# Kernel tuning notes

Hardware: AMD Instinct MI355X
Metric: run time of the kernel (lower is better)

## Reference

```python
import jax, jax.numpy as jnp
import numpy as np
import math

B, TQ, TK = 64, 1024, 512
CONV_CH, EMBED_DIM, ATT_HID = 512, 512, 512
KEY_POS_RATE = 1.385
QUERY_POS_RATE = 1.0
POSITION_WEIGHT = 1.0


def sin_pos_enc(positions, w, d):
    # positions: [B, T] int, padding_idx=0 maps to zero vector.
    # pe[..., 2i]   = sin(w*pos / 10000^(2i/d))
    # pe[..., 2i+1] = cos(w*pos / 10000^(2i/d))
    i = jnp.arange(d)
    inv_freq = jnp.power(jnp.float32(10000.0), -(2.0 * (i // 2).astype(jnp.float32)) / d)  # [d]
    ang = (positions.astype(jnp.float32) * w)[..., None] * inv_freq  # [B, T, d]
    pe = jnp.where(i % 2 == 0, jnp.sin(ang), jnp.cos(ang))
    return jnp.where((positions == 0)[..., None], jnp.float32(0.0), pe)


def setup_inputs() -> dict:
    key = jax.random.key(0)
    ks = jax.random.split(key, 12)
    s = 0.02
    inp = {
        "query": jax.random.normal(ks[0], (B, TQ, CONV_CH), jnp.float32),
        "keys": jax.random.normal(ks[1], (B, TK, EMBED_DIM), jnp.float32),
        "values": jax.random.normal(ks[2], (B, TK, EMBED_DIM), jnp.float32),
        # 1-based positions (0 is the padding index of SinusoidalEncoding)
        "text_positions": jnp.broadcast_to(jnp.arange(1, TK + 1, dtype=jnp.int64), (B, TK)),
        "frame_positions": jnp.broadcast_to(jnp.arange(1, TQ + 1, dtype=jnp.int64), (B, TQ)),
        # pad mask over keys: last 64 text positions are padding
        "mask": jnp.broadcast_to(jnp.arange(TK) >= (TK - 64), (B, TK)),
        "Wq": jax.random.normal(ks[3], (CONV_CH, ATT_HID), jnp.float32) * s,
        "bq": jnp.zeros((ATT_HID,), jnp.float32),
        "Wk": jax.random.normal(ks[4], (EMBED_DIM, ATT_HID), jnp.float32) * s,
        "bk": jnp.zeros((ATT_HID,), jnp.float32),
        "Wv": jax.random.normal(ks[5], (EMBED_DIM, ATT_HID), jnp.float32) * s,
        "bv": jnp.zeros((ATT_HID,), jnp.float32),
        "Wo": jax.random.normal(ks[6], (ATT_HID, CONV_CH), jnp.float32) * s,
        "bo": jnp.zeros((CONV_CH,), jnp.float32),
    }
    return inp


def reference(query, keys, values, text_positions, frame_positions, mask,
              Wq, bq, Wk, bk, Wv, bv, Wo, bo):
    # positional-bias injection (position_weight = 1.0)
    keys = keys + POSITION_WEIGHT * sin_pos_enc(text_positions, KEY_POS_RATE, EMBED_DIM)[:, :keys.shape[1], :]
    query = query + POSITION_WEIGHT * sin_pos_enc(frame_positions, QUERY_POS_RATE, CONV_CH)[:, :frame_positions.shape[-1], :]

    v = values @ Wv + bv            # [B, TK, H]
    k = keys @ Wk + bk              # [B, TK, H]
    q = query @ Wq + bq             # [B, TQ, H]

    scores = jnp.einsum('bqh,bkh->bqk', q, k)               # [B, TQ, TK]
    scores = jnp.where(mask[:, None, :], -jnp.inf, scores)
    attn = jax.nn.softmax(scores, axis=2)
    # dropout is a no-op in eval mode
    x = jnp.einsum('bqk,bkh->bqh', attn, v)
    x = x * jnp.float32(math.sqrt(1.0 / v.shape[1]))
    out = x @ Wo + bo               # [B, TQ, conv_channels]
    return out, attn
```

## Files before the change

kernel.cpp:

```cpp
#include <hip/hip_runtime.h>
#include <stdint.h>

#define DEVI __device__ __forceinline__

typedef __attribute__((ext_vector_type(4))) float     f4v;
typedef __attribute__((ext_vector_type(8))) _Float16  h8;
typedef __attribute__((ext_vector_type(4))) _Float16  h4;
typedef unsigned int  u32;

static constexpr int   TQ = 1024, TKN = 512;
static constexpr float KEY_RATE = 1.385f;
static constexpr float QRY_RATE = 1.0f;
static constexpr float SCALE    = 0.04419417382415922f;
static constexpr float INVC     = 0.05190512648261504f;

static constexpr size_t OFF_MM   = 0;
static constexpr size_t OFF_NT   = OFF_MM  + (size_t)512*512*2;
static constexpr size_t OFF_WOT  = OFF_NT  + (size_t)512*512*2;
static constexpr size_t OFF_PEQ  = OFF_WOT + (size_t)512*512*4;
static constexpr size_t OFF_W    = OFF_PEQ + (size_t)1024*512*4;
static constexpr size_t OFF_C    = OFF_W   + 2048;
static constexpr size_t OFF_BQBK = OFF_C   + 2048;
static constexpr size_t OFF_T    = OFF_BQBK + 256;
static constexpr size_t OFF_KP   = OFF_T   + (size_t)64*512*4;
static constexpr size_t OFF_MKT  = OFF_KP  + (size_t)64*512*512*2;
static constexpr size_t OFF_PT   = OFF_MKT + (size_t)64*512*512*2;
static constexpr size_t WS_NEED  = OFF_PT  + (size_t)64*512*512*2;
static constexpr size_t OFF_A16  = WS_NEED;
static constexpr size_t WS_BIG   = OFF_A16 + (size_t)64*1024*512*2;

#define WAITV(N) asm volatile("s_waitcnt vmcnt(" #N ")" ::: "memory")
#define WAITL()  asm volatile("s_waitcnt lgkmcnt(0)" ::: "memory")
#define SCHEDB() __builtin_amdgcn_sched_barrier(0)
#define BARRAW() __builtin_amdgcn_s_barrier()

DEVI f4v mfma16(h8 a, h8 b, f4v c) {
  return __builtin_amdgcn_mfma_f32_16x16x32_f16(a, b, c, 0, 0, 0);
}

DEVI void gld16(void* lds, const void* g) {
  __builtin_amdgcn_global_load_lds(
      (const __attribute__((address_space(1))) unsigned int*)g,
      (__attribute__((address_space(3))) unsigned int*)lds, 16, 0, 0);
}

DEVI void stage_B(char* Bbuf, const _Float16* B, int k0, int tid) {
#pragma unroll
  for (int it = 0; it < 4; ++it) {
    const int c = (it << 9) + tid;
    const int r = c >> 2, s = c & 3;
    const int sg = s ^ ((r >> 1) & 3);
    gld16(Bbuf + ((size_t)c << 4), B + (size_t)r * 512 + k0 + (sg << 3));
  }
}

DEVI void stage_A16(char* Abuf, const _Float16* A, int k0, int tid) {
  const int r = tid >> 2, s = tid & 3;
  const int sg = s ^ ((r >> 1) & 3);
  gld16(Abuf + ((size_t)tid << 4), A + (size_t)r * 512 + k0 + (sg << 3));
}

DEVI void loads_A32(f4v& x0, f4v& x1, const float* A, const float* add, int k0, int tid) {
  const int r = tid >> 2, c8 = (tid & 3) << 3;
  const float* p = A + (size_t)r * 512 + k0 + c8;
  x0 = *(const f4v*)p; x1 = *(const f4v*)(p + 4);
  if (add) {
    const float* q = add + (size_t)r * 512 + k0 + c8;
    x0 += *(const f4v*)q; x1 += *(const f4v*)(q + 4);
  }
}
DEVI void write_A32(char* Abuf, f4v x0, f4v x1, int tid) {
  const int r = tid >> 2;
  const int slot = (tid & 3) ^ ((r >> 1) & 3);
  h8 o;
#pragma unroll
  for (int i = 0; i < 4; ++i) { o[i] = (_Float16)x0[i]; o[4 + i] = (_Float16)x1[i]; }
  *(h8*)(Abuf + (r << 6) + (slot << 4)) = o;
}

DEVI void read_fragsA(const char* Ab, int wr, int lane, h8 (&a)[4]) {
  const int l15 = lane & 15, hi = lane >> 4;
#pragma unroll
  for (int mi = 0; mi < 4; ++mi) {
    const int r = wr * 64 + mi * 16 + l15;
    a[mi] = *(const h8*)(Ab + (r << 6) + ((hi ^ ((r >> 1) & 3)) << 4));
  }
}
DEVI void read_fragsB(const char* Bb, int wc, int lane, h8 (&b)[8]) {
  const int l15 = lane & 15, hi = lane >> 4;
#pragma unroll
  for (int nj = 0; nj < 8; ++nj) {
    const int g = wc * 128 + nj * 16 + l15;
    b[nj] = *(const h8*)(Bb + (g << 6) + ((hi ^ ((g >> 1) & 3)) << 4));
  }
}

#define MFMA_ALL(a, bf, acc) do {                               \
  __builtin_amdgcn_s_setprio(1);                                \
  _Pragma("unroll") for (int mi = 0; mi < 4; ++mi)              \
  _Pragma("unroll") for (int nj = 0; nj < 8; ++nj)              \
      acc[mi][nj] = mfma16(a[mi], bf[nj], acc[mi][nj]);         \
  __builtin_amdgcn_s_setprio(0);                                \
} while (0)

#define REG_PIPELINE(As, Ad, Bs, acc)                                              \
  {                                                                                \
    char* const Abf[2] = {lds, lds + 8192};                                        \
    char* const Bbf[3] = {lds + 16384, lds + 49152, lds + 81920};                  \
    f4v xa0, xa1, xb0, xb1;                                                        \
    loads_A32(xa0, xa1, As, Ad, 0, tid);                                           \
    loads_A32(xb0, xb1, As, Ad, 32, tid);                                          \
    SCHEDB();                                                                      \
    stage_B(Bbf[0], Bs, 0, tid);                                                   \
    stage_B(Bbf[1], Bs, 32, tid);                                                  \
    WAITV(4);                                                                      \
    write_A32(Abf[0], xa0, xa1, tid);                                              \
    WAITL(); SCHEDB(); BARRAW(); SCHEDB();                                         \
    _Pragma("unroll")                                                              \
    for (int k = 0; k < 16; ++k) {                                                 \
      if (k < 14) {                                                                \
        if ((k & 1) == 0) { loads_A32(xa0, xa1, As, Ad, (k + 2) * 32, tid); }      \
        else              { loads_A32(xb0, xb1, As, Ad, (k + 2) * 32, tid); }      \
        SCHEDB();                                                                  \
        stage_B(Bbf[(k + 2) % 3], Bs, (k + 2) * 32, tid);                          \
      }                                                                            \
      h8 a[4], bf[8];                                                              \
      read_fragsA(Abf[k & 1], wr, lane, a);                                        \
      read_fragsB(Bbf[k % 3], wc, lane, bf);                                       \
      MFMA_ALL(a, bf, acc);                                                        \
      if (k < 15) {                                                                \
        if (k < 14) { WAITV(6); } else { WAITV(0); }                               \
        if ((k & 1) == 0) write_A32(Abf[1], xb0, xb1, tid);                        \
        else              write_A32(Abf[0], xa0, xa1, tid);                        \
        WAITL(); SCHEDB(); BARRAW(); SCHEDB();                                     \
      }                                                                            \
    }                                                                              \
  }

#define GLD_PIPELINE(As, Bs, acc)                                                  \
  {                                                                                \
    char* const Abf[3] = {lds, lds + 8192, lds + 16384};                           \
    char* const Bbf[3] = {lds + 24576, lds + 57344, lds + 90112};                  \
    stage_A16(Abf[0], As, 0, tid);  stage_B(Bbf[0], Bs, 0, tid);                   \
    stage_A16(Abf[1], As, 32, tid); stage_B(Bbf[1], Bs, 32, tid);                  \
    WAITV(5); SCHEDB(); BARRAW(); SCHEDB();                                        \
    _Pragma("unroll")                                                              \
    for (int k = 0; k < 16; ++k) {                                                 \
      if (k < 14) {                                                                \
        stage_A16(Abf[(k + 2) % 3], As, (k + 2) * 32, tid);                        \
        stage_B(Bbf[(k + 2) % 3], Bs, (k + 2) * 32, tid);                          \
      }                                                                            \
      h8 a[4], bf[8];                                                              \
      read_fragsA(Abf[k % 3], wr, lane, a);                                        \
      read_fragsB(Bbf[k % 3], wc, lane, bf);                                       \
      MFMA_ALL(a, bf, acc);                                                        \
      if (k < 14) { WAITV(5); } else if (k == 14) { WAITV(0); }                    \
      if (k < 15) { WAITL(); SCHEDB(); BARRAW(); SCHEDB(); }                       \
    }                                                                              \
  }

DEVI void stage_f32_A(char* Abuf, const float* A, int k0, int tid) {
#pragma unroll
  for (int it = 0; it < 2; ++it) {
    const int idx = (it << 9) + tid;
    const int r = idx >> 3, c4 = idx & 7;
    f4v x = *(const f4v*)(A + (size_t)r * 512 + k0 + (c4 << 2));
    h4 o;
#pragma unroll
    for (int i = 0; i < 4; ++i) o[i] = (_Float16)x[i];
    const int slot = (c4 >> 1) ^ ((r >> 1) & 3);
    *(h4*)(Abuf + (r << 6) + (slot << 4) + ((c4 & 1) << 3)) = o;
  }
}
DEVI void stage_f32_B(char* Bbuf, const float* B, int k0, int tid) {
#pragma unroll
  for (int it = 0; it < 8; ++it) {
    const int idx = (it << 9) + tid;
    const int r = idx >> 3, c4 = idx & 7;
    f4v x = *(const f4v*)(B + (size_t)r * 512 + k0 + (c4 << 2));
    h4 o;
#pragma unroll
    for (int i = 0; i < 4; ++i) o[i] = (_Float16)x[i];
    const int slot = (c4 >> 1) ^ ((r >> 1) & 3);
    *(h4*)(Bbuf + (r << 6) + (slot << 4) + ((c4 & 1) << 3)) = o;
  }
}

__global__ __launch_bounds__(256) void k_prepA(
    const float* __restrict__ Wk, const float* __restrict__ bq,
    const float* __restrict__ bk,
    const float* __restrict__ Wo,
    const void* __restrict__ fpos_raw,
    float* __restrict__ wvec, float* __restrict__ bqbk,
    float* __restrict__ PEQ, float* __restrict__ WoT) {
  const int bid = blockIdx.x, tid = threadIdx.x;
  if (bid < 128) {
    const int wid = tid >> 6, lane = tid & 63;
    const int row = bid * 4 + wid;
    const float* p = Wk + (size_t)row * 512 + lane * 8;
    const f4v a = *(const f4v*)p, c = *(const f4v*)(p + 4);
    const f4v b0 = *(const f4v*)(bq + lane * 8), b1 = *(const f4v*)(bq + lane * 8 + 4);
    float d = a[0]*b0[0]+a[1]*b0[1]+a[2]*b0[2]+a[3]*b0[3]
            + c[0]*b1[0]+c[1]*b1[1]+c[2]*b1[2]+c[3]*b1[3];
#pragma unroll
    for (int off = 32; off; off >>= 1) d += __shfl_xor(d, off);
    if (lane == 0) wvec[row] = d;
  } else if (bid == 128) {
    __shared__ float red[256];
    red[tid] = bq[tid] * bk[tid] + bq[tid + 256] * bk[tid + 256];
    __syncthreads();
    if (tid == 0) { float s = 0.f; for (int h = 0; h < 256; ++h) s += red[h]; bqbk[0] = s; }
  } else if (bid < 129 + 2048) {
    const u32* fp = (const u32*)fpos_raw;
    const bool is64 = (fp[1] == 0);
    const int t = (bid - 129) * 256 + tid;
    const int tq = t >> 9, d = t & 511;
    const int pos = (int)(is64 ? fp[2 * tq] : fp[tq]);
    float pe = 0.f;
    if (pos != 0) {
      const float invf = exp2f(-(float)(d >> 1) * INVC);
      const float ang  = ((float)pos * QRY_RATE) * invf;
      pe = (d & 1) ? cosf(ang) : sinf(ang);
    }
    PEQ[t] = pe;
  } else {
    __shared__ float t[32][33];
    const int local = bid - 2177;
    const int bx = local & 15, by = local >> 4;
    const int tx = tid & 31, ty = tid >> 5;
    const int x = bx * 32 + tx;
#pragma unroll
    for (int j = 0; j < 4; ++j)
      t[ty + 8 * j][tx] = Wo[(size_t)(by * 32 + ty + 8 * j) * 512 + x];
    __syncthreads();
    const int x2 = by * 32 + tx;
#pragma unroll
    for (int j = 0; j < 4; ++j)
      WoT[(size_t)(bx * 32 + ty + 8 * j) * 512 + x2] = t[tx][ty + 8 * j];
  }
}

__global__ __launch_bounds__(512) void k_prepB(
    const float* __restrict__ Wq, const float* __restrict__ Wk,
    const float* __restrict__ WoT, const float* __restrict__ Wv,
    const float* __restrict__ keys, const void* __restrict__ tpos_raw,
    const void* __restrict__ mask_raw,
    const float* __restrict__ wvec, const float* __restrict__ bqbk,
    const float* __restrict__ bv, const float* __restrict__ bo,
    _Float16* __restrict__ Mm, _Float16* __restrict__ Nt,
    _Float16* __restrict__ kp, float* __restrict__ tvec,
    float* __restrict__ cvec) {
  __shared__ char lds[40960];
  const int bid = blockIdx.x, tid = threadIdx.x;
  const int lane = tid & 63, wid = tid >> 6;
  if (bid < 8) {
    char *Ab = lds, *Bb = lds + 8192;
    const int wr = wid >> 2, wc = wid & 3;
    const int x = bid & 3, y = bid >> 2;
    const float* A = (y == 0 ? Wq : WoT) + (size_t)x * 128 * 512;
    const float* B = (y == 0 ? Wk : Wv);
    _Float16* out = (y == 0 ? Mm : Nt) + (size_t)x * 128 * 512;
    f4v acc[4][8] = {};
    for (int ks = 0; ks < 16; ++ks) {
      stage_f32_A(Ab, A, ks * 32, tid);
      stage_f32_B(Bb, B, ks * 32, tid);
      __syncthreads();
      h8 a[4], bf[8];
      read_fragsA(Ab, wr, lane, a);
      read_fragsB(Bb, wc, lane, bf);
      MFMA_ALL(a, bf, acc);
      __syncthreads();
    }
    const int l15 = lane & 15, hi = lane >> 4;
#pragma unroll
    for (int mi = 0; mi < 4; ++mi)
#pragma unroll
      for (int nj = 0; nj < 8; ++nj) {
        const int col = wc * 128 + nj * 16 + l15;
#pragma unroll
        for (int j = 0; j < 4; ++j) {
          const int row = wr * 64 + mi * 16 + hi * 4 + j;
          out[(size_t)row * 512 + col] = (_Float16)acc[mi][nj][j];
        }
      }
  } else if (bid < 4104) {
    const u32* tp = (const u32*)tpos_raw;
    const bool is64 = (tp[1] == 0);
    const int row = (bid - 8) * 8 + wid;
    const int pos = (int)(is64 ? tp[2 * row] : tp[row]);
    const int d0  = lane * 8;
    const float* src = keys + (size_t)row * 512 + d0;
    const f4v a = *(const f4v*)src, b = *(const f4v*)(src + 4);
    float x[8] = {a[0], a[1], a[2], a[3], b[0], b[1], b[2], b[3]};
    if (pos != 0) {
      const float pw = (float)pos * KEY_RATE;
#pragma unroll
      for (int u = 0; u < 4; ++u) {
        const float invf = exp2f(-(float)(lane * 4 + u) * INVC);
        const float ang  = pw * invf;
        x[2*u]   += sinf(ang);
        x[2*u+1] += cosf(ang);
      }
    }
    const f4v w0 = *(const f4v*)(wvec + d0), w1 = *(const f4v*)(wvec + d0 + 4);
    float dot = 0.f;
#pragma unroll
    for (int i = 0; i < 4; ++i) dot += x[i] * w0[i] + x[4+i] * w1[i];
#pragma unroll
    for (int off = 32; off; off >>= 1) dot += __shfl_xor(dot, off);
    if (lane == 0) {
      const u32* m32 = (const u32*)mask_raw;
      const bool is32 = (m32[448] != 0);
      const bool mk = is32 ? (m32[row] != 0)
                           : (((const unsigned char*)mask_raw)[row] != 0);
      tvec[row] = mk ? -1e30f : (dot + bqbk[0]);
    }
    h8 o;
#pragma unroll
    for (int i = 0; i < 8; ++i) o[i] = (_Float16)x[i];
    *(h8*)(kp + (size_t)row * 512 + d0) = o;
  } else {
    const int row = (bid - 4104) * 8 + wid;
    const float* p = WoT + (size_t)row * 512 + lane * 8;
    const f4v a = *(const f4v*)p, c = *(const f4v*)(p + 4);
    const f4v b0 = *(const f4v*)(bv + lane * 8), b1 = *(const f4v*)(bv + lane * 8 + 4);
    float d = a[0]*b0[0]+a[1]*b0[1]+a[2]*b0[2]+a[3]*b0[3]
            + c[0]*b1[0]+c[1]*b1[1]+c[2]*b1[2]+c[3]*b1[3];
#pragma unroll
    for (int off = 32; off; off >>= 1) d += __shfl_xor(d, off);
    if (lane == 0) cvec[row] = SCALE * d + bo[row];
  }
}

__global__ __launch_bounds__(512, 1) void k_mkpv(
    const _Float16* __restrict__ kp, const _Float16* __restrict__ Mm,
    const float* __restrict__ values, const _Float16* __restrict__ Nt,
    _Float16* __restrict__ MKt, _Float16* __restrict__ Pt) {
  __shared__ char lds[122880];
  const int bid = blockIdx.x, tid = threadIdx.x;
  const int lane = tid & 63, wid = tid >> 6;
  const int wr = wid >> 2, wc = wid & 3;
  const int l15 = lane & 15, hi = lane >> 4;
  f4v acc[4][8] = {};
  if (bid < 256) {
    const int tt = bid & 3, b = bid >> 2;
    const _Float16* As = kp + ((size_t)b * TKN + tt * 128) * 512;
    GLD_PIPELINE(As, Mm, acc);
    _Float16* Ob = MKt + (size_t)b * TKN * 512 + (size_t)tt * 128 * 512;
#pragma unroll
    for (int mi = 0; mi < 4; ++mi)
#pragma unroll
      for (int nj = 0; nj < 8; ++nj) {
        const int col = wc * 128 + nj * 16 + l15;
#pragma unroll
        for (int j = 0; j < 4; ++j) {
          const int row = wr * 64 + mi * 16 + hi * 4 + j;
          Ob[(size_t)row * 512 + col] = (_Float16)acc[mi][nj][j];
        }
      }
  } else {
    const int rt = (bid - 256) & 3, b = (bid - 256) >> 2;
    const float* As = values + ((size_t)b * TKN + rt * 128) * 512;
    const float* Ad = nullptr;
    REG_PIPELINE(As, Ad, Nt, acc);
    _Float16* Pb = Pt + (size_t)b * 512 * 512;
#pragma unroll
    for (int mi = 0; mi < 4; ++mi)
#pragma unroll
      for (int nj = 0; nj < 8; ++nj) {
        const int col = wc * 128 + nj * 16 + l15;
        const int t0  = rt * 128 + wr * 64 + mi * 16 + hi * 4;
        h4 o;
#pragma unroll
        for (int j = 0; j < 4; ++j) o[j] = (_Float16)acc[mi][nj][j];
        *(h4*)(Pb + (size_t)col * 512 + t0) = o;
      }
  }
}

__global__ __launch_bounds__(512, 1) void k_scores(
    const float* __restrict__ query, const float* __restrict__ PEQ,
    const _Float16* __restrict__ MKt, const float* __restrict__ tve,
    float* __restrict__ attn, _Float16* __restrict__ a16) {
  __shared__ char lds[114688];
  const int tid = threadIdx.x, lane = tid & 63, wid = tid >> 6;
  const int wr = wid >> 2, wc = wid & 3;
  const int bid = blockIdx.x;
  const int xcd = bid & 7, i = bid >> 3;
  const int qt = i & 7, b = xcd * 8 + (i >> 3);
  const float* As = query + ((size_t)b * TQ + qt * 128) * 512;
  const float* Ad = PEQ + (size_t)(qt * 128) * 512;
  const _Float16* Bs = MKt + (size_t)b * TKN * 512;
  const int l15 = lane & 15, hi = lane >> 4;
  float tv[8];
#pragma unroll
  for (int nj = 0; nj < 8; ++nj) tv[nj] = tve[b * TKN + wc * 128 + nj * 16 + l15];
  f4v acc[4][8] = {};
  REG_PIPELINE(As, Ad, Bs, acc);
  float* red  = (float*)lds;
  float* red2 = (float*)(lds + 2048);
#pragma unroll
  for (int mi = 0; mi < 4; ++mi)
#pragma unroll
    for (int nj = 0; nj < 8; ++nj) {
      const float t = tv[nj];
#pragma unroll
      for (int j = 0; j < 4; ++j) acc[mi][nj][j] += t;
    }
  float mrow[4][4];
#pragma unroll
  for (int mi = 0; mi < 4; ++mi)
#pragma unroll
    for (int j = 0; j < 4; ++j) {
      float m = acc[mi][0][j];
#pragma unroll
      for (int nj = 1; nj < 8; ++nj) m = fmaxf(m, acc[mi][nj][j]);
      m = fmaxf(m, __shfl_xor(m, 1)); m = fmaxf(m, __shfl_xor(m, 2));
      m = fmaxf(m, __shfl_xor(m, 4)); m = fmaxf(m, __shfl_xor(m, 8));
      mrow[mi][j] = m;
    }
  __syncthreads();
  if (l15 == 0) {
#pragma unroll
    for (int mi = 0; mi < 4; ++mi)
#pragma unroll
      for (int j = 0; j < 4; ++j)
        red[(wr * 64 + mi * 16 + hi * 4 + j) * 4 + wc] = mrow[mi][j];
  }
  __syncthreads();
#pragma unroll
  for (int mi = 0; mi < 4; ++mi)
#pragma unroll
    for (int j = 0; j < 4; ++j) {
      const f4v rv = *(const f4v*)(red + (wr * 64 + mi * 16 + hi * 4 + j) * 4);
      mrow[mi][j] = fmaxf(fmaxf(rv[0], rv[1]), fmaxf(rv[2], rv[3]));
    }
  float srow[4][4];
#pragma unroll
  for (int mi = 0; mi < 4; ++mi)
#pragma unroll
    for (int j = 0; j < 4; ++j) {
      float s = 0.f;
      const float m = mrow[mi][j];
#pragma unroll
      for (int nj = 0; nj < 8; ++nj) {
        const float e = expf(acc[mi][nj][j] - m);
        acc[mi][nj][j] = e; s += e;
      }
      s += __shfl_xor(s, 1); s += __shfl_xor(s, 2);
      s += __shfl_xor(s, 4); s += __shfl_xor(s, 8);
      srow[mi][j] = s;
    }
  if (l15 == 0) {
#pragma unroll
    for (int mi = 0; mi < 4; ++mi)
#pragma unroll
      for (int j = 0; j < 4; ++j)
        red2[(wr * 64 + mi * 16 + hi * 4 + j) * 4 + wc] = srow[mi][j];
  }
  __syncthreads();
  float* Ao = attn + ((size_t)b * TQ + qt * 128) * 512;
  _Float16* Ah = a16 ? a16 + ((size_t)b * TQ + qt * 128) * 512 : nullptr;
#pragma unroll
  for (int mi = 0; mi < 4; ++mi)
#pragma unroll
    for (int j = 0; j < 4; ++j) {
      const int row = wr * 64 + mi * 16 + hi * 4 + j;
      const f4v sv = *(const f4v*)(red2 + row * 4);
      const float rinv = 1.f / (sv[0] + sv[1] + sv[2] + sv[3]);
#pragma unroll
      for (int nj = 0; nj < 8; ++nj) {
        const float v = acc[mi][nj][j] * rinv;
        const int col = wc * 128 + nj * 16 + l15;
        Ao[(size_t)row * 512 + col] = v;
        if (Ah) Ah[(size_t)row * 512 + col] = (_Float16)v;
      }
    }
}

template <int A16P>
__global__ __launch_bounds__(512, 1) void k_final(
    const float* __restrict__ attn, const _Float16* __restrict__ attn16,
    const _Float16* __restrict__ Pt, const float* __restrict__ cvec,
    float* __restrict__ outp) {
  __shared__ char lds[122880];
  const int tid = threadIdx.x, lane = tid & 63, wid = tid >> 6;
  const int wr = wid >> 2, wc = wid & 3;
  const int bid = blockIdx.x;
  const int xcd = bid & 7, i = bid >> 3;
  const int qt = i & 7, b = xcd * 8 + (i >> 3);
  const _Float16* Bs = Pt + (size_t)b * 512 * 512;
  const int l15 = lane & 15, hi = lane >> 4;
  f4v acc[4][8] = {};
  if (A16P) {
    const _Float16* As = attn16 + ((size_t)b * TQ + qt * 128) * 512;
    GLD_PIPELINE(As, Bs, acc);
  } else {
    const float* As = attn + ((size_t)b * TQ + qt * 128) * 512;
    const float* Ad = nullptr;
    REG_PIPELINE(As, Ad, Bs, acc);
  }
  float cv[8];
#pragma unroll
  for (int nj = 0; nj < 8; ++nj) cv[nj] = cvec[wc * 128 + nj * 16 + l15];
  float* Ob = outp + ((size_t)b * TQ + qt * 128) * 512;
#pragma unroll
  for (int mi = 0; mi < 4; ++mi)
#pragma unroll
    for (int nj = 0; nj < 8; ++nj) {
      const int col = wc * 128 + nj * 16 + l15;
#pragma unroll
      for (int j = 0; j < 4; ++j) {
        const int row = wr * 64 + mi * 16 + hi * 4 + j;
        Ob[(size_t)row * 512 + col] = SCALE * acc[mi][nj][j] + cv[nj];
      }
    }
}

extern "C" void kernel_launch(void* const* d_in, const int* in_sizes, int n_in,
                              void* d_out, int out_size, void* d_ws, size_t ws_size,
                              hipStream_t stream) {
  (void)in_sizes; (void)n_in; (void)out_size;
  if (ws_size < WS_NEED) return;
  const bool big = (ws_size >= WS_BIG);

  const float* query  = (const float*)d_in[0];
  const float* keys   = (const float*)d_in[1];
  const float* values = (const float*)d_in[2];
  const void*  tpos   = d_in[3];
  const void*  fpos   = d_in[4];
  const void*  mask   = d_in[5];
  const float* Wq = (const float*)d_in[6];
  const float* bq = (const float*)d_in[7];
  const float* Wk = (const float*)d_in[8];
  const float* bk = (const float*)d_in[9];
  const float* Wv = (const float*)d_in[10];
  const float* bv = (const float*)d_in[11];
  const float* Wo = (const float*)d_in[12];
  const float* bo = (const float*)d_in[13];

  char* ws = (char*)d_ws;
  _Float16* Mm   = (_Float16*)(ws + OFF_MM);
  _Float16* Nt   = (_Float16*)(ws + OFF_NT);
  float*    WoT  = (float*)   (ws + OFF_WOT);
  float*    PEQ  = (float*)   (ws + OFF_PEQ);
  float*    wvec = (float*)   (ws + OFF_W);
  float*    cvec = (float*)   (ws + OFF_C);
  float*    bqbk = (float*)   (ws + OFF_BQBK);
  float*    tvec = (float*)   (ws + OFF_T);
  _Float16* kp   = (_Float16*)(ws + OFF_KP);
  _Float16* MKt  = (_Float16*)(ws + OFF_MKT);
  _Float16* Pt   = (_Float16*)(ws + OFF_PT);
  _Float16* a16  = big ? (_Float16*)(ws + OFF_A16) : nullptr;

  float* outp = (float*)d_out;
  float* attn = outp + (size_t)64 * TQ * 512;

  k_prepA<<<2433, 256, 0, stream>>>(Wk, bq, bk, Wo, fpos, wvec, bqbk, PEQ, WoT);
  k_prepB<<<4168, 512, 0, stream>>>(Wq, Wk, WoT, Wv, keys, tpos, mask,
                                    wvec, bqbk, bv, bo, Mm, Nt, kp, tvec, cvec);
  k_mkpv <<<512, 512, 0, stream>>>(kp, Mm, values, Nt, MKt, Pt);
  k_scores<<<512, 512, 0, stream>>>(query, PEQ, MKt, tvec, attn, a16);
  if (big) k_final<1><<<512, 512, 0, stream>>>(attn, a16, Pt, cvec, outp);
  else     k_final<0><<<512, 512, 0, stream>>>(attn, a16, Pt, cvec, outp);
}
```

Before: 300.1 us.

## Halve GEMM block tiles and double grid to raise occupancy

Shrinks the per-block tiles of the mkpv, scores and final GEMM kernels from 128x512 to 128x256 (mkpv and final, with the column half chosen by block index) and to 64x512 (scores, with eight waves splitting columns). LDS use falls to 72KB, launch bounds allow more blocks per CU, and each grid grows to 1024 blocks. The aim is more concurrent waves to hide memory latency and fill the CUs better. In exchange, operand tiles are re-fetched more often, the scores softmax now reduces across 8 waves per row, and the pipeline wait counts are retuned by hand, which risks ordering errors.

```diff
diff --git a/kernel.cpp b/kernel.cpp
--- a/kernel.cpp
+++ b/kernel.cpp
@@ -44,7 +44,7 @@
       (__attribute__((address_space(3))) unsigned int*)lds, 16, 0, 0);
 }
 
-DEVI void stage_B(char* Bbuf, const _Float16* B, int k0, int tid) {
+DEVI void stage_B512(char* Bbuf, const _Float16* B, int k0, int tid) {
 #pragma unroll
   for (int it = 0; it < 4; ++it) {
     const int c = (it << 9) + tid;
@@ -53,7 +53,15 @@
     gld16(Bbuf + ((size_t)c << 4), B + (size_t)r * 512 + k0 + (sg << 3));
   }
 }
-
+DEVI void stage_B256(char* Bbuf, const _Float16* B, int k0, int tid) {
+#pragma unroll
+  for (int it = 0; it < 2; ++it) {
+    const int c = (it << 9) + tid;
+    const int r = c >> 2, s = c & 3;
+    const int sg = s ^ ((r >> 1) & 3);
+    gld16(Bbuf + ((size_t)c << 4), B + (size_t)r * 512 + k0 + (sg << 3));
+  }
+}
 DEVI void stage_A16(char* Abuf, const _Float16* A, int k0, int tid) {
   const int r = tid >> 2, s = tid & 3;
   const int sg = s ^ ((r >> 1) & 3);
@@ -77,6 +85,19 @@
   for (int i = 0; i < 4; ++i) { o[i] = (_Float16)x0[i]; o[4 + i] = (_Float16)x1[i]; }
   *(h8*)(Abuf + (r << 6) + (slot << 4)) = o;
 }
+DEVI void loads_A64(f4v& x, const float* A, const float* add, int k0, int tid) {
+  const int r = tid >> 3, c4 = tid & 7;
+  x = *(const f4v*)(A + (size_t)r * 512 + k0 + (c4 << 2));
+  if (add) x += *(const f4v*)(add + (size_t)r * 512 + k0 + (c4 << 2));
+}
+DEVI void write_A64(char* Abuf, f4v x, int tid) {
+  const int r = tid >> 3, c4 = tid & 7;
+  h4 o;
+#pragma unroll
+  for (int i = 0; i < 4; ++i) o[i] = (_Float16)x[i];
+  const int slot = (c4 >> 1) ^ ((r >> 1) & 3);
+  *(h4*)(Abuf + (r << 6) + (slot << 4) + ((c4 & 1) << 3)) = o;
+}
 
 DEVI void read_fragsA(const char* Ab, int wr, int lane, h8 (&a)[4]) {
   const int l15 = lane & 15, hi = lane >> 4;
@@ -86,7 +107,15 @@
     a[mi] = *(const h8*)(Ab + (r << 6) + ((hi ^ ((r >> 1) & 3)) << 4));
   }
 }
-DEVI void read_fragsB(const char* Bb, int wc, int lane, h8 (&b)[8]) {
+DEVI void read_fragsB4(const char* Bb, int cb, int lane, h8 (&b)[4]) {
+  const int l15 = lane & 15, hi = lane >> 4;
+#pragma unroll
+  for (int nj = 0; nj < 4; ++nj) {
+    const int g = cb + nj * 16 + l15;
+    b[nj] = *(const h8*)(Bb + (g << 6) + ((hi ^ ((g >> 1) & 3)) << 4));
+  }
+}
+DEVI void read_fragsB8(const char* Bb, int wc, int lane, h8 (&b)[8]) {
   const int l15 = lane & 15, hi = lane >> 4;
 #pragma unroll
   for (int nj = 0; nj < 8; ++nj) {
@@ -95,66 +124,73 @@
   }
 }
 
-#define MFMA_ALL(a, bf, acc) do {                               \
+#define MFMA_ALL4(a, bf, acc) do {                              \
   __builtin_amdgcn_s_setprio(1);                                \
+  _Pragma("unroll") for (int mi = 0; mi < 4; ++mi)              \
+  _Pragma("unroll") for (int nj = 0; nj < 4; ++nj)              \
+      acc[mi][nj] = mfma16(a[mi], bf[nj], acc[mi][nj]);         \
+  __builtin_amdgcn_s_setprio(0);                                \
+} while (0)
+
+#define MFMA_ALL8(a, bf, acc) do {                              \
   _Pragma("unroll") for (int mi = 0; mi < 4; ++mi)              \
   _Pragma("unroll") for (int nj = 0; nj < 8; ++nj)              \
       acc[mi][nj] = mfma16(a[mi], bf[nj], acc[mi][nj]);         \
-  __builtin_amdgcn_s_setprio(0);                                \
 } while (0)
 
-#define REG_PIPELINE(As, Ad, Bs, acc)                                              \
+#define REG256_PIPELINE(As, Ad, Bs, acc)                                           \
   {                                                                                \
     char* const Abf[2] = {lds, lds + 8192};                                        \
-    char* const Bbf[3] = {lds + 16384, lds + 49152, lds + 81920};                  \
+    char* const Bbf[3] = {lds + 16384, lds + 32768, lds + 49152};                  \
     f4v xa0, xa1, xb0, xb1;                                                        \
     loads_A32(xa0, xa1, As, Ad, 0, tid);                                           \
     loads_A32(xb0, xb1, As, Ad, 32, tid);                                          \
     SCHEDB();                                                                      \
-    stage_B(Bbf[0], Bs, 0, tid);                                                   \
-    stage_B(Bbf[1], Bs, 32, tid);                                                  \
-    WAITV(4);                                                                      \
+    stage_B256(Bbf[0], Bs, 0, tid);                                                \
+    stage_B256(Bbf[1], Bs, 32, tid);                                               \
+    WAITV(6);                                                                      \
     write_A32(Abf[0], xa0, xa1, tid);                                              \
-    WAITL(); SCHEDB(); BARRAW(); SCHEDB();                                         \
+    WAITV(2); WAITL(); SCHEDB(); BARRAW(); SCHEDB();                               \
     _Pragma("unroll")                                                              \
     for (int k = 0; k < 16; ++k) {                                                 \
       if (k < 14) {                                                                \
         if ((k & 1) == 0) { loads_A32(xa0, xa1, As, Ad, (k + 2) * 32, tid); }      \
         else              { loads_A32(xb0, xb1, As, Ad, (k + 2) * 32, tid); }      \
         SCHEDB();                                                                  \
-        stage_B(Bbf[(k + 2) % 3], Bs, (k + 2) * 32, tid);                          \
+        stage_B256(Bbf[(k + 2) % 3], Bs, (k + 2) * 32, tid);                       \
       }                                                                            \
-      h8 a[4], bf[8];                                                              \
+      h8 a[4], bf[4];                                                              \
       read_fragsA(Abf[k & 1], wr, lane, a);                                        \
-      read_fragsB(Bbf[k % 3], wc, lane, bf);                                       \
-      MFMA_ALL(a, bf, acc);                                                        \
+      read_fragsB4(Bbf[k % 3], wc * 64, lane, bf);                                 \
+      MFMA_ALL4(a, bf, acc);                                                       \
       if (k < 15) {                                                                \
-        if (k < 14) { WAITV(6); } else { WAITV(0); }                               \
+        if (k < 14) { WAITV(4); } else { WAITV(2); }                               \
         if ((k & 1) == 0) write_A32(Abf[1], xb0, xb1, tid);                        \
         else              write_A32(Abf[0], xa0, xa1, tid);                        \
+        if (k == 14) { WAITV(0); }                                                 \
         WAITL(); SCHEDB(); BARRAW(); SCHEDB();                                     \
       }                                                                            \
     }                                                                              \
   }
 
-#define GLD_PIPELINE(As, Bs, acc)                                                  \
+#define GLD256_PIPELINE(As, Bs, acc)                                               \
   {                                                                                \
     char* const Abf[3] = {lds, lds + 8192, lds + 16384};                           \
-    char* const Bbf[3] = {lds + 24576, lds + 57344, lds + 90112};                  \
-    stage_A16(Abf[0], As, 0, tid);  stage_B(Bbf[0], Bs, 0, tid);                   \
-    stage_A16(Abf[1], As, 32, tid); stage_B(Bbf[1], Bs, 32, tid);                  \
-    WAITV(5); SCHEDB(); BARRAW(); SCHEDB();                                        \
+    char* const Bbf[3] = {lds + 24576, lds + 40960, lds + 57344};                  \
+    stage_A16(Abf[0], As, 0, tid);  stage_B256(Bbf[0], Bs, 0, tid);                \
+    stage_A16(Abf[1], As, 32, tid); stage_B256(Bbf[1], Bs, 32, tid);               \
+    WAITV(3); SCHEDB(); BARRAW(); SCHEDB();                                        \
     _Pragma("unroll")                                                              \
     for (int k = 0; k < 16; ++k) {                                                 \
       if (k < 14) {                                                                \
         stage_A16(Abf[(k + 2) % 3], As, (k + 2) * 32, tid);                        \
-        stage_B(Bbf[(k + 2) % 3], Bs, (k + 2) * 32, tid);                          \
+        stage_B256(Bbf[(k + 2) % 3], Bs, (k + 2) * 32, tid);                       \
       }                                                                            \
-      h8 a[4], bf[8];                                                              \
+      h8 a[4], bf[4];                                                              \
       read_fragsA(Abf[k % 3], wr, lane, a);                                        \
-      read_fragsB(Bbf[k % 3], wc, lane, bf);                                       \
-      MFMA_ALL(a, bf, acc);                                                        \
-      if (k < 14) { WAITV(5); } else if (k == 14) { WAITV(0); }                    \
+      read_fragsB4(Bbf[k % 3], wc * 64, lane, bf);                                 \
+      MFMA_ALL4(a, bf, acc);                                                       \
+      if (k < 14) { WAITV(3); } else if (k == 14) { WAITV(0); }                    \
       if (k < 15) { WAITL(); SCHEDB(); BARRAW(); SCHEDB(); }                       \
     }                                                                              \
   }
@@ -267,8 +303,8 @@
       __syncthreads();
       h8 a[4], bf[8];
       read_fragsA(Ab, wr, lane, a);
-      read_fragsB(Bb, wc, lane, bf);
-      MFMA_ALL(a, bf, acc);
+      read_fragsB8(Bb, wc, lane, bf);
+      MFMA_ALL8(a, bf, acc);
       __syncthreads();
     }
     const int l15 = lane & 15, hi = lane >> 4;
@@ -332,26 +368,27 @@
   }
 }
 
-__global__ __launch_bounds__(512, 1) void k_mkpv(
+__global__ __launch_bounds__(512, 4) void k_mkpv(
     const _Float16* __restrict__ kp, const _Float16* __restrict__ Mm,
     const float* __restrict__ values, const _Float16* __restrict__ Nt,
     _Float16* __restrict__ MKt, _Float16* __restrict__ Pt) {
-  __shared__ char lds[122880];
+  __shared__ char lds[73728];
   const int bid = blockIdx.x, tid = threadIdx.x;
   const int lane = tid & 63, wid = tid >> 6;
   const int wr = wid >> 2, wc = wid & 3;
   const int l15 = lane & 15, hi = lane >> 4;
-  f4v acc[4][8] = {};
-  if (bid < 256) {
-    const int tt = bid & 3, b = bid >> 2;
+  f4v acc[4][4] = {};
+  if (bid < 512) {
+    const int nt = bid & 1, tt = (bid >> 1) & 3, b = bid >> 3;
     const _Float16* As = kp + ((size_t)b * TKN + tt * 128) * 512;
-    GLD_PIPELINE(As, Mm, acc);
+    const _Float16* Bs = Mm + (size_t)nt * 256 * 512;
+    GLD256_PIPELINE(As, Bs, acc);
     _Float16* Ob = MKt + (size_t)b * TKN * 512 + (size_t)tt * 128 * 512;
 #pragma unroll
     for (int mi = 0; mi < 4; ++mi)
 #pragma unroll
-      for (int nj = 0; nj < 8; ++nj) {
-        const int col = wc * 128 + nj * 16 + l15;
+      for (int nj = 0; nj < 4; ++nj) {
+        const int col = nt * 256 + wc * 64 + nj * 16 + l15;
 #pragma unroll
         for (int j = 0; j < 4; ++j) {
           const int row = wr * 64 + mi * 16 + hi * 4 + j;
@@ -359,16 +396,18 @@
         }
       }
   } else {
-    const int rt = (bid - 256) & 3, b = (bid - 256) >> 2;
+    const int idx = bid - 512;
+    const int nt = idx & 1, rt = (idx >> 1) & 3, b = idx >> 3;
     const float* As = values + ((size_t)b * TKN + rt * 128) * 512;
     const float* Ad = nullptr;
-    REG_PIPELINE(As, Ad, Nt, acc);
+    const _Float16* Bs = Nt + (size_t)nt * 256 * 512;
+    REG256_PIPELINE(As, Ad, Bs, acc);
     _Float16* Pb = Pt + (size_t)b * 512 * 512;
 #pragma unroll
     for (int mi = 0; mi < 4; ++mi)
 #pragma unroll
-      for (int nj = 0; nj < 8; ++nj) {
-        const int col = wc * 128 + nj * 16 + l15;
+      for (int nj = 0; nj < 4; ++nj) {
+        const int col = nt * 256 + wc * 64 + nj * 16 + l15;
         const int t0  = rt * 128 + wr * 64 + mi * 16 + hi * 4;
         h4 o;
 #pragma unroll
@@ -378,137 +417,173 @@
   }
 }
 
-__global__ __launch_bounds__(512, 1) void k_scores(
+__global__ __launch_bounds__(512, 4) void k_scores(
     const float* __restrict__ query, const float* __restrict__ PEQ,
     const _Float16* __restrict__ MKt, const float* __restrict__ tve,
     float* __restrict__ attn, _Float16* __restrict__ a16) {
-  __shared__ char lds[114688];
+  __shared__ char lds[73728];
+  const int tid = threadIdx.x, lane = tid & 63, wc = tid >> 6;
+  const int bid = blockIdx.x;
+  const int xcd = bid & 7, i = bid >> 3;
+  const int qt = i & 15, b = xcd * 8 + (i >> 4);
+  const float* As = query + ((size_t)b * TQ + qt * 64) * 512;
+  const float* Ad = PEQ + (size_t)(qt * 64) * 512;
+  const _Float16* Bs = MKt + (size_t)b * TKN * 512;
+  const int l15 = lane & 15, hi = lane >> 4;
+  float tv[4];
+#pragma unroll
+  for (int nj = 0; nj < 4; ++nj) tv[nj] = tve[b * TKN + wc * 64 + nj * 16 + l15];
+
+  f4v acc[4][4] = {};
+  {
+    char* const Abf[2] = {lds, lds + 4096};
+    char* const Bbf[2] = {lds + 8192, lds + 40960};
+    f4v xa, xb;
+    loads_A64(xa, As, Ad, 0, tid);
+    SCHEDB();
+    stage_B512(Bbf[0], Bs, 0, tid);
+    loads_A64(xb, As, Ad, 32, tid);
+    WAITV(5);
+    write_A64(Abf[0], xa, tid);
+    WAITV(1);
+    WAITL(); SCHEDB(); BARRAW(); SCHEDB();
+#pragma unroll
+    for (int k = 0; k < 16; ++k) {
+      if (k < 15) stage_B512(Bbf[(k + 1) & 1], Bs, (k + 1) * 32, tid);
+      if (k < 14) {
+        if ((k & 1) == 0) { loads_A64(xa, As, Ad, (k + 2) * 32, tid); }
+        else              { loads_A64(xb, As, Ad, (k + 2) * 32, tid); }
+      }
+      h8 a[4], bf[4];
+      read_fragsA(Abf[k & 1], 0, lane, a);
+      read_fragsB4(Bbf[k & 1], wc * 64, lane, bf);
+      MFMA_ALL4(a, bf, acc);
+      if (k < 15) {
+        if (k < 14) { WAITV(5); } else { WAITV(4); }
+        if ((k & 1) == 0) write_A64(Abf[1], xb, tid);
+        else              write_A64(Abf[0], xa, tid);
+        if (k < 14) { WAITV(1); } else { WAITV(0); }
+        WAITL(); SCHEDB(); BARRAW(); SCHEDB();
+      }
+    }
+  }
+
+  float* red  = (float*)lds;
+  float* red2 = (float*)(lds + 2048);
+#pragma unroll
+  for (int mi = 0; mi < 4; ++mi)
+#pragma unroll
+    for (int nj = 0; nj < 4; ++nj) {
+      const float t = tv[nj];
+#pragma unroll
+      for (int j = 0; j < 4; ++j) acc[mi][nj][j] += t;
+    }
+  float mrow[4][4];
+#pragma unroll
+  for (int mi = 0; mi < 4; ++mi)
+#pragma unroll
+    for (int j = 0; j < 4; ++j) {
+      float m = acc[mi][0][j];
+#pragma unroll
+      for (int nj = 1; nj < 4; ++nj) m = fmaxf(m, acc[mi][nj][j]);
+      m = fmaxf(m, __shfl_xor(m, 1)); m = fmaxf(m, __shfl_xor(m, 2));
+      m = fmaxf(m, __shfl_xor(m, 4)); m = fmaxf(m, __shfl_xor(m, 8));
+      mrow[mi][j] = m;
+    }
+  if (l15 == 0) {
+#pragma unroll
+    for (int mi = 0; mi < 4; ++mi)
+#pragma unroll
+      for (int j = 0; j < 4; ++j)
+        red[(mi * 16 + hi * 4 + j) * 8 + wc] = mrow[mi][j];
+  }
+  __syncthreads();
+#pragma unroll
+  for (int mi = 0; mi < 4; ++mi)
+#pragma unroll
+    for (int j = 0; j < 4; ++j) {
+      const int row = mi * 16 + hi * 4 + j;
+      const f4v r0 = *(const f4v*)(red + row * 8);
+      const f4v r1 = *(const f4v*)(red + row * 8 + 4);
+      mrow[mi][j] = fmaxf(fmaxf(fmaxf(r0[0], r0[1]), fmaxf(r0[2], r0[3])),
+                          fmaxf(fmaxf(r1[0], r1[1]), fmaxf(r1[2], r1[3])));
+    }
+  float srow[4][4];
+#pragma unroll
+  for (int mi = 0; mi < 4; ++mi)
+#pragma unroll
+    for (int j = 0; j < 4; ++j) {
+      float s = 0.f;
+      const float m = mrow[mi][j];
+#pragma unroll
+      for (int nj = 0; nj < 4; ++nj) {
+        const float e = expf(acc[mi][nj][j] - m);
+        acc[mi][nj][j] = e; s += e;
+      }
+      s += __shfl_xor(s, 1); s += __shfl_xor(s, 2);
+      s += __shfl_xor(s, 4); s += __shfl_xor(s, 8);
+      srow[mi][j] = s;
+    }
+  if (l15 == 0) {
+#pragma unroll
+    for (int mi = 0; mi < 4; ++mi)
+#pragma unroll
+      for (int j = 0; j < 4; ++j)
+        red2[(mi * 16 + hi * 4 + j) * 8 + wc] = srow[mi][j];
+  }
+  __syncthreads();
+  float* Ao = attn + ((size_t)b * TQ + qt * 64) * 512;
+  _Float16* Ah = a16 ? a16 + ((size_t)b * TQ + qt * 64) * 512 : nullptr;
+#pragma unroll
+  for (int mi = 0; mi < 4; ++mi)
+#pragma unroll
+    for (int j = 0; j < 4; ++j) {
+      const int row = mi * 16 + hi * 4 + j;
+      const f4v s0 = *(const f4v*)(red2 + row * 8);
+      const f4v s1 = *(const f4v*)(red2 + row * 8 + 4);
+      const float rinv = 1.f / (s0[0] + s0[1] + s0[2] + s0[3] +
+                                s1[0] + s1[1] + s1[2] + s1[3]);
+#pragma unroll
+      for (int nj = 0; nj < 4; ++nj) {
+        const float v = acc[mi][nj][j] * rinv;
+        const int col = wc * 64 + nj * 16 + l15;
+        Ao[(size_t)row * 512 + col] = v;
+        if (Ah) Ah[(size_t)row * 512 + col] = (_Float16)v;
+      }
+    }
+}
+
+template <int A16P>
+__global__ __launch_bounds__(512, 4) void k_final(
+    const float* __restrict__ attn, const _Float16* __restrict__ attn16,
+    const _Float16* __restrict__ Pt, const float* __restrict__ cvec,
+    float* __restrict__ outp) {
+  __shared__ char lds[73728];
   const int tid = threadIdx.x, lane = tid & 63, wid = tid >> 6;
   const int wr = wid >> 2, wc = wid & 3;
   const int bid = blockIdx.x;
   const int xcd = bid & 7, i = bid >> 3;
-  const int qt = i & 7, b = xcd * 8 + (i >> 3);
-  const float* As = query + ((size_t)b * TQ + qt * 128) * 512;
-  const float* Ad = PEQ + (size_t)(qt * 128) * 512;
-  const _Float16* Bs = MKt + (size_t)b * TKN * 512;
+  const int qt = i & 7, nt = (i >> 3) & 1, b = xcd * 8 + (i >> 4);
+  const _Float16* Bs = Pt + (size_t)b * 512 * 512 + (size_t)nt * 256 * 512;
   const int l15 = lane & 15, hi = lane >> 4;
-  float tv[8];
-#pragma unroll
-  for (int nj = 0; nj < 8; ++nj) tv[nj] = tve[b * TKN + wc * 128 + nj * 16 + l15];
-  f4v acc[4][8] = {};
-  REG_PIPELINE(As, Ad, Bs, acc);
-  float* red  = (float*)lds;
-  float* red2 = (float*)(lds + 2048);
-#pragma unroll
-  for (int mi = 0; mi < 4; ++mi)
-#pragma unroll
-    for (int nj = 0; nj < 8; ++nj) {
-      const float t = tv[nj];
-#pragma unroll
-      for (int j = 0; j < 4; ++j) acc[mi][nj][j] += t;
-    }
-  float mrow[4][4];
-#pragma unroll
-  for (int mi = 0; mi < 4; ++mi)
-#pragma unroll
-    for (int j = 0; j < 4; ++j) {
-      float m = acc[mi][0][j];
-#pragma unroll
-      for (int nj = 1; nj < 8; ++nj) m = fmaxf(m, acc[mi][nj][j]);
-      m = fmaxf(m, __shfl_xor(m, 1)); m = fmaxf(m, __shfl_xor(m, 2));
-      m = fmaxf(m, __shfl_xor(m, 4)); m = fmaxf(m, __shfl_xor(m, 8));
-      mrow[mi][j] = m;
-    }
-  __syncthreads();
-  if (l15 == 0) {
-#pragma unroll
-    for (int mi = 0; mi < 4; ++mi)
-#pragma unroll
-      for (int j = 0; j < 4; ++j)
-        red[(wr * 64 + mi * 16 + hi * 4 + j) * 4 + wc] = mrow[mi][j];
-  }
-  __syncthreads();
-#pragma unroll
-  for (int mi = 0; mi < 4; ++mi)
-#pragma unroll
-    for (int j = 0; j < 4; ++j) {
-      const f4v rv = *(const f4v*)(red + (wr * 64 + mi * 16 + hi * 4 + j) * 4);
-      mrow[mi][j] = fmaxf(fmaxf(rv[0], rv[1]), fmaxf(rv[2], rv[3]));
-    }
-  float srow[4][4];
-#pragma unroll
-  for (int mi = 0; mi < 4; ++mi)
-#pragma unroll
-    for (int j = 0; j < 4; ++j) {
-      float s = 0.f;
-      const float m = mrow[mi][j];
-#pragma unroll
-      for (int nj = 0; nj < 8; ++nj) {
-        const float e = expf(acc[mi][nj][j] - m);
-        acc[mi][nj][j] = e; s += e;
-      }
-      s += __shfl_xor(s, 1); s += __shfl_xor(s, 2);
-      s += __shfl_xor(s, 4); s += __shfl_xor(s, 8);
-      srow[mi][j] = s;
-    }
-  if (l15 == 0) {
-#pragma unroll
-    for (int mi = 0; mi < 4; ++mi)
-#pragma unroll
-      for (int j = 0; j < 4; ++j)
-        red2[(wr * 64 + mi * 16 + hi * 4 + j) * 4 + wc] = srow[mi][j];
-  }
-  __syncthreads();
-  float* Ao = attn + ((size_t)b * TQ + qt * 128) * 512;
-  _Float16* Ah = a16 ? a16 + ((size_t)b * TQ + qt * 128) * 512 : nullptr;
-#pragma unroll
-  for (int mi = 0; mi < 4; ++mi)
-#pragma unroll
-    for (int j = 0; j < 4; ++j) {
-      const int row = wr * 64 + mi * 16 + hi * 4 + j;
-      const f4v sv = *(const f4v*)(red2 + row * 4);
-      const float rinv = 1.f / (sv[0] + sv[1] + sv[2] + sv[3]);
-#pragma unroll
-      for (int nj = 0; nj < 8; ++nj) {
-        const float v = acc[mi][nj][j] * rinv;
-        const int col = wc * 128 + nj * 16 + l15;
-        Ao[(size_t)row * 512 + col] = v;
-        if (Ah) Ah[(size_t)row * 512 + col] = (_Float16)v;
-      }
-    }
-}
-
-template <int A16P>
-__global__ __launch_bounds__(512, 1) void k_final(
-    const float* __restrict__ attn, const _Float16* __restrict__ attn16,
-    const _Float16* __restrict__ Pt, const float* __restrict__ cvec,
-    float* __restrict__ outp) {
-  __shared__ char lds[122880];
-  const int tid = threadIdx.x, lane = tid & 63, wid = tid >> 6;
-  const int wr = wid >> 2, wc = wid & 3;
-  const int bid = blockIdx.x;
-  const int xcd = bid & 7, i = bid >> 3;
-  const int qt = i & 7, b = xcd * 8 + (i >> 3);
-  const _Float16* Bs = Pt + (size_t)b * 512 * 512;
-  const int l15 = lane & 15, hi = lane >> 4;
-  f4v acc[4][8] = {};
+  f4v acc[4][4] = {};
   if (A16P) {
     const _Float16* As = attn16 + ((size_t)b * TQ + qt * 128) * 512;
-    GLD_PIPELINE(As, Bs, acc);
+    GLD256_PIPELINE(As, Bs, acc);
   } else {
     const float* As = attn + ((size_t)b * TQ + qt * 128) * 512;
     const float* Ad = nullptr;
-    REG_PIPELINE(As, Ad, Bs, acc);
-  }
-  float cv[8];
-#pragma unroll
-  for (int nj = 0; nj < 8; ++nj) cv[nj] = cvec[wc * 128 + nj * 16 + l15];
+    REG256_PIPELINE(As, Ad, Bs, acc);
+  }
+  float cv[4];
+#pragma unroll
+  for (int nj = 0; nj < 4; ++nj) cv[nj] = cvec[nt * 256 + wc * 64 + nj * 16 + l15];
   float* Ob = outp + ((size_t)b * TQ + qt * 128) * 512;
 #pragma unroll
   for (int mi = 0; mi < 4; ++mi)
 #pragma unroll
-    for (int nj = 0; nj < 8; ++nj) {
-      const int col = wc * 128 + nj * 16 + l15;
+    for (int nj = 0; nj < 4; ++nj) {
+      const int col = nt * 256 + wc * 64 + nj * 16 + l15;
 #pragma unroll
       for (int j = 0; j < 4; ++j) {
         const int row = wr * 64 + mi * 16 + hi * 4 + j;
@@ -559,8 +634,8 @@
   k_prepA<<<2433, 256, 0, stream>>>(Wk, bq, bk, Wo, fpos, wvec, bqbk, PEQ, WoT);
   k_prepB<<<4168, 512, 0, stream>>>(Wq, Wk, WoT, Wv, keys, tpos, mask,
                                     wvec, bqbk, bv, bo, Mm, Nt, kp, tvec, cvec);
-  k_mkpv <<<512, 512, 0, stream>>>(kp, Mm, values, Nt, MKt, Pt);
-  k_scores<<<512, 512, 0, stream>>>(query, PEQ, MKt, tvec, attn, a16);
-  if (big) k_final<1><<<512, 512, 0, stream>>>(attn, a16, Pt, cvec, outp);
-  else     k_final<0><<<512, 512, 0, stream>>>(attn, a16, Pt, cvec, outp);
-}
+  k_mkpv <<<1024, 512, 0, stream>>>(kp, Mm, values, Nt, MKt, Pt);
+  k_scores<<<1024, 512, 0, stream>>>(query, PEQ, MKt, tvec, attn, a16);
+  if (big) k_final<1><<<1024, 512, 0, stream>>>(attn, a16, Pt, cvec, outp);
+  else     k_final<0><<<1024, 512, 0, stream>>>(attn, a16, Pt, cvec, outp);
+}
```

Measured after the change: 346.9 us. 15.6% more time.

## Process two K-steps per barrier with four-deep LDS buffers in GEMM pipelines

Applied to the files above, without the earlier changes.

Both GEMM pipelines now use four LDS buffers for A and B and handle two 32-wide K slices between barriers, so there are half as many barriers and wait points. The register and global-load prefetch now fetches two slices at a time and waits for all outstanding loads (WAITV(0)) before each barrier instead of keeping a partial wait. LDS per block grows to 160 KB, which the MI355X's larger LDS allows. The cost is less fine-grained overlap, since all loads must finish before each barrier, and higher LDS use.

```diff
diff --git a/kernel.cpp b/kernel.cpp
--- a/kernel.cpp
+++ b/kernel.cpp
@@ -105,33 +105,39 @@
 
 #define REG_PIPELINE(As, Ad, Bs, acc)                                              \
   {                                                                                \
-    char* const Abf[2] = {lds, lds + 8192};                                        \
-    char* const Bbf[3] = {lds + 16384, lds + 49152, lds + 81920};                  \
+    char* const Abf[4] = {lds, lds + 8192, lds + 16384, lds + 24576};              \
+    char* const Bbf[4] = {lds + 32768, lds + 65536, lds + 98304, lds + 131072};    \
     f4v xa0, xa1, xb0, xb1;                                                        \
+    stage_B(Bbf[0], Bs, 0, tid);                                                   \
+    stage_B(Bbf[1], Bs, 32, tid);                                                  \
     loads_A32(xa0, xa1, As, Ad, 0, tid);                                           \
     loads_A32(xb0, xb1, As, Ad, 32, tid);                                          \
     SCHEDB();                                                                      \
-    stage_B(Bbf[0], Bs, 0, tid);                                                   \
-    stage_B(Bbf[1], Bs, 32, tid);                                                  \
-    WAITV(4);                                                                      \
+    WAITV(0);                                                                      \
     write_A32(Abf[0], xa0, xa1, tid);                                              \
+    write_A32(Abf[1], xb0, xb1, tid);                                              \
     WAITL(); SCHEDB(); BARRAW(); SCHEDB();                                         \
     _Pragma("unroll")                                                              \
-    for (int k = 0; k < 16; ++k) {                                                 \
-      if (k < 14) {                                                                \
-        if ((k & 1) == 0) { loads_A32(xa0, xa1, As, Ad, (k + 2) * 32, tid); }      \
-        else              { loads_A32(xb0, xb1, As, Ad, (k + 2) * 32, tid); }      \
+    for (int p = 0; p < 8; ++p) {                                                  \
+      const int s0 = 2 * p, s1 = 2 * p + 1;                                        \
+      if (p < 7) {                                                                 \
+        stage_B(Bbf[(s0 + 2) & 3], Bs, (s0 + 2) * 32, tid);                        \
+        stage_B(Bbf[(s1 + 2) & 3], Bs, (s1 + 2) * 32, tid);                        \
+        loads_A32(xa0, xa1, As, Ad, (s0 + 2) * 32, tid);                           \
+        loads_A32(xb0, xb1, As, Ad, (s1 + 2) * 32, tid);                           \
         SCHEDB();                                                                  \
-        stage_B(Bbf[(k + 2) % 3], Bs, (k + 2) * 32, tid);                          \
       }                                                                            \
       h8 a[4], bf[8];                                                              \
-      read_fragsA(Abf[k & 1], wr, lane, a);                                        \
-      read_fragsB(Bbf[k % 3], wc, lane, bf);                                       \
+      read_fragsA(Abf[s0 & 3], wr, lane, a);                                       \
+      read_fragsB(Bbf[s0 & 3], wc, lane, bf);                                      \
       MFMA_ALL(a, bf, acc);                                                        \
-      if (k < 15) {                                                                \
-        if (k < 14) { WAITV(6); } else { WAITV(0); }                               \
-        if ((k & 1) == 0) write_A32(Abf[1], xb0, xb1, tid);                        \
-        else              write_A32(Abf[0], xa0, xa1, tid);                        \
+      read_fragsA(Abf[s1 & 3], wr, lane, a);                                       \
+      read_fragsB(Bbf[s1 & 3], wc, lane, bf);                                      \
+      MFMA_ALL(a, bf, acc);                                                        \
+      if (p < 7) {                                                                 \
+        WAITV(0);                                                                  \
+        write_A32(Abf[(s0 + 2) & 3], xa0, xa1, tid);                               \
+        write_A32(Abf[(s1 + 2) & 3], xb0, xb1, tid);                               \
         WAITL(); SCHEDB(); BARRAW(); SCHEDB();                                     \
       }                                                                            \
     }                                                                              \
@@ -139,23 +145,28 @@
 
 #define GLD_PIPELINE(As, Bs, acc)                                                  \
   {                                                                                \
-    char* const Abf[3] = {lds, lds + 8192, lds + 16384};                           \
-    char* const Bbf[3] = {lds + 24576, lds + 57344, lds + 90112};                  \
+    char* const Abf[4] = {lds, lds + 8192, lds + 16384, lds + 24576};              \
+    char* const Bbf[4] = {lds + 32768, lds + 65536, lds + 98304, lds + 131072};    \
     stage_A16(Abf[0], As, 0, tid);  stage_B(Bbf[0], Bs, 0, tid);                   \
     stage_A16(Abf[1], As, 32, tid); stage_B(Bbf[1], Bs, 32, tid);                  \
-    WAITV(5); SCHEDB(); BARRAW(); SCHEDB();                                        \
+    WAITV(0); SCHEDB(); BARRAW(); SCHEDB();                                        \
     _Pragma("unroll")                                                              \
-    for (int k = 0; k < 16; ++k) {                                                 \
-      if (k < 14) {                                                                \
-        stage_A16(Abf[(k + 2) % 3], As, (k + 2) * 32, tid);                        \
-        stage_B(Bbf[(k + 2) % 3], Bs, (k + 2) * 32, tid);                          \
+    for (int p = 0; p < 8; ++p) {                                                  \
+      const int s0 = 2 * p, s1 = 2 * p + 1;                                        \
+      if (p < 7) {                                                                 \
+        stage_A16(Abf[(s0 + 2) & 3], As, (s0 + 2) * 32, tid);                      \
+        stage_B(Bbf[(s0 + 2) & 3], Bs, (s0 + 2) * 32, tid);                        \
+        stage_A16(Abf[(s1 + 2) & 3], As, (s1 + 2) * 32, tid);                      \
+        stage_B(Bbf[(s1 + 2) & 3], Bs, (s1 + 2) * 32, tid);                        \
       }                                                                            \
       h8 a[4], bf[8];                                                              \
-      read_fragsA(Abf[k % 3], wr, lane, a);                                        \
-      read_fragsB(Bbf[k % 3], wc, lane, bf);                                       \
+      read_fragsA(Abf[s0 & 3], wr, lane, a);                                       \
+      read_fragsB(Bbf[s0 & 3], wc, lane, bf);                                      \
       MFMA_ALL(a, bf, acc);                                                        \
-      if (k < 14) { WAITV(5); } else if (k == 14) { WAITV(0); }                    \
-      if (k < 15) { WAITL(); SCHEDB(); BARRAW(); SCHEDB(); }                       \
+      read_fragsA(Abf[s1 & 3], wr, lane, a);                                       \
+      read_fragsB(Bbf[s1 & 3], wc, lane, bf);                                      \
+      MFMA_ALL(a, bf, acc);                                                        \
+      if (p < 7) { WAITV(0); WAITL(); SCHEDB(); BARRAW(); SCHEDB(); }              \
     }                                                                              \
   }
 
@@ -336,7 +347,7 @@
     const _Float16* __restrict__ kp, const _Float16* __restrict__ Mm,
     const float* __restrict__ values, const _Float16* __restrict__ Nt,
     _Float16* __restrict__ MKt, _Float16* __restrict__ Pt) {
-  __shared__ char lds[122880];
+  __shared__ char lds[163840];
   const int bid = blockIdx.x, tid = threadIdx.x;
   const int lane = tid & 63, wid = tid >> 6;
   const int wr = wid >> 2, wc = wid & 3;
@@ -382,7 +393,7 @@
     const float* __restrict__ query, const float* __restrict__ PEQ,
     const _Float16* __restrict__ MKt, const float* __restrict__ tve,
     float* __restrict__ attn, _Float16* __restrict__ a16) {
-  __shared__ char lds[114688];
+  __shared__ char lds[163840];
   const int tid = threadIdx.x, lane = tid & 63, wid = tid >> 6;
   const int wr = wid >> 2, wc = wid & 3;
   const int bid = blockIdx.x;
@@ -483,7 +494,7 @@
     const float* __restrict__ attn, const _Float16* __restrict__ attn16,
     const _Float16* __restrict__ Pt, const float* __restrict__ cvec,
     float* __restrict__ outp) {
-  __shared__ char lds[122880];
+  __shared__ char lds[163840];
   const int tid = threadIdx.x, lane = tid & 63, wid = tid >> 6;
   const int wr = wid >> 2, wc = wid & 3;
   const int bid = blockIdx.x;
```

Measured after the change: 316.1 us. 5.3% more time.
